# Kernel optimization log

Measured on AMD Instinct MI355X. Metric: run time of the kernel, lower is better.

The kernel has to match this reference:

```python
import jax, jax.numpy as jnp
import numpy as np
from jax import lax

B, P, ENC, H, A, E, V, TC = 64, 196, 2048, 1024, 1024, 512, 10000, 32


def setup_inputs() -> dict:
    key = jax.random.key(0)
    ks = jax.random.split(key, 24)
    s = 0.02
    inp = {
        'enc_out': jax.random.normal(ks[0], (B, P, ENC), jnp.float32),
        'enc_captions': jax.random.randint(ks[1], (B, TC), 0, V),
        'lengths': jax.random.randint(ks[2], (B,), 2, TC + 1).at[0].set(TC),
        'W_enc_att': jax.random.normal(ks[3], (A, ENC)) * s,
        'b_enc_att': jnp.zeros((A,)),
        'W_dec_att': jax.random.normal(ks[4], (A, H)) * s,
        'b_dec_att': jnp.zeros((A,)),
        'W_full': jax.random.normal(ks[5], (1, A)) * s,
        'b_full': jnp.zeros((1,)),
        'emb': jax.random.uniform(ks[6], (V, E), minval=-0.1, maxval=0.1),
        'W_ih': jax.random.normal(ks[7], (4 * H, E + ENC)) * s,
        'b_ih': jnp.zeros((4 * H,)),
        'W_hh': jax.random.normal(ks[8], (4 * H, H)) * s,
        'b_hh': jnp.zeros((4 * H,)),
        'W_init_h': jax.random.normal(ks[9], (H, ENC)) * s,
        'b_init_h': jnp.zeros((H,)),
        'W_init_c': jax.random.normal(ks[10], (H, ENC)) * s,
        'b_init_c': jnp.zeros((H,)),
        'W_beta': jax.random.normal(ks[11], (ENC, H)) * s,
        'b_beta': jnp.zeros((ENC,)),
        'W_fc': jax.random.uniform(ks[12], (V, H), minval=-0.1, maxval=0.1),
        'b_fc': jnp.zeros((V,)),
    }
    return inp


def reference(enc_out, enc_captions, lengths,
              W_enc_att, b_enc_att, W_dec_att, b_dec_att, W_full, b_full,
              emb, W_ih, b_ih, W_hh, b_hh,
              W_init_h, b_init_h, W_init_c, b_init_c,
              W_beta, b_beta, W_fc, b_fc):
    T = enc_captions.shape[1] - 1  # static max decode length (setup forces one full-length row)
    ind = jnp.argsort(-lengths)
    lens = lengths[ind]
    eo = enc_out[ind]              # [B,P,ENC] sorted by length desc
    caps = enc_captions[ind]
    dec_lens = lens - 1
    embs = emb[caps]               # [B,TC,E]

    mean_a = eo.mean(axis=1)
    h0 = mean_a @ W_init_h.T + b_init_h
    c0 = mean_a @ W_init_c.T + b_init_c

    # encoder projection is time-invariant; hoist out of the loop
    enc_att = jnp.einsum('bpe,ae->bpa', eo, W_enc_att) + b_enc_att  # [B,P,A]

    mask_ts = jnp.arange(T)[:, None] < dec_lens[None, :]            # [T,B]
    emb_ts = jnp.swapaxes(embs[:, :T, :], 0, 1)                     # [T,B,E]

    def step(carry, xs):
        h, c = carry
        emb_t, m = xs  # [B,E], [B] bool (active rows = leading batch_size_t)
        # attention
        dec = h @ W_dec_att.T + b_dec_att                            # [B,A]
        a = jax.nn.relu(enc_att + dec[:, None, :]) @ W_full[0] + b_full[0]  # [B,P]
        alpha = jax.nn.softmax(a, axis=1)
        context = jnp.einsum('bpe,bp->be', eo, alpha)                # [B,ENC]
        # gate + LSTM cell (torch gate order: i, f, g, o)
        gate = jax.nn.sigmoid(h @ W_beta.T + b_beta)
        awe = gate * context
        x = jnp.concatenate([emb_t, awe], axis=1)
        gates = x @ W_ih.T + b_ih + h @ W_hh.T + b_hh
        i, f, g, o = jnp.split(gates, 4, axis=1)
        c_new = jax.nn.sigmoid(f) * c + jax.nn.sigmoid(i) * jnp.tanh(g)
        h_new = jax.nn.sigmoid(o) * jnp.tanh(c_new)
        m2 = m[:, None]
        h2 = jnp.where(m2, h_new, h)  # inactive rows keep frozen state
        c2 = jnp.where(m2, c_new, c)
        mf = m2.astype(h.dtype)
        preds = (h_new @ W_fc.T + b_fc) * mf  # dropout = identity (eval)
        return (h2, c2), (preds, alpha * mf)

    (_, _), (preds, alphas) = lax.scan(step, (h0, c0), (emb_ts, mask_ts))
    predictions = jnp.swapaxes(preds, 0, 1)   # [B,T,V]
    alphas = jnp.swapaxes(alphas, 0, 1)       # [B,T,P]
    return predictions, alphas, caps, dec_lens, ind
```

## Files before the change

kernel.cpp:

```cpp
#include <hip/hip_runtime.h>

#define Bn   64
#define Pp   196
#define ENCd 2048
#define Hd   1024
#define Ad   1024
#define Ed   512
#define Vd   10000
#define TCd  32
#define Td   31
#define XHW  3584
#define VPAD 10240

typedef short bf16x8 __attribute__((ext_vector_type(8)));
typedef float f32x4  __attribute__((ext_vector_type(4)));

static __device__ __forceinline__ float bf2f(unsigned short u) {
    unsigned int x = ((unsigned int)u) << 16;
    float f; __builtin_memcpy(&f, &x, 4); return f;
}
static __device__ __forceinline__ unsigned short f2bf(float f) {
    unsigned int x; __builtin_memcpy(&x, &f, 4);
    x += 0x7fffu + ((x >> 16) & 1u);
    return (unsigned short)(x >> 16);
}
static __device__ __forceinline__ float sigf(float x) { return 1.f / (1.f + expf(-x)); }


__global__ void sort_kernel(const int* __restrict__ lengths, const int* __restrict__ captions,
                            int* __restrict__ ind, int* __restrict__ dl,
                            float* __restrict__ out_caps, float* __restrict__ out_dl,
                            float* __restrict__ out_ind) {
    __shared__ int s_ind[Bn];
    int tid = threadIdx.x;
    int Lt = lengths[tid];
    int pos = 0;
    for (int k = 0; k < Bn; ++k) {
        int Lk = lengths[k];
        pos += (Lk > Lt) || (Lk == Lt && k < tid);
    }
    s_ind[pos] = tid;
    __syncthreads();
    int src = s_ind[tid];
    ind[tid] = src;
    int d = lengths[src] - 1;
    dl[tid] = d;
    out_ind[tid] = (float)src;
    out_dl[tid] = (float)d;
    for (int j = 0; j < TCd; ++j)
        out_caps[tid * TCd + j] = (float)captions[src * TCd + j];
}

__global__ void cvt_kernel(const float* __restrict__ src, unsigned short* __restrict__ dst, int n) {
    int i = blockIdx.x * 256 + threadIdx.x;
    int stride = gridDim.x * 256;
    for (; i < n; i += stride) dst[i] = f2bf(src[i]);
}

__global__ void wcat_kernel(const float* __restrict__ wih, const float* __restrict__ whh,
                            unsigned short* __restrict__ wcat) {
    int j = blockIdx.y;
    int idx = blockIdx.x * 256 + threadIdx.x;
    float v = (idx < 2560) ? wih[(size_t)j * 2560 + idx] : whh[(size_t)j * 1024 + (idx - 2560)];
    wcat[(size_t)j * XHW + idx] = f2bf(v);
}

__global__ void biascat_kernel(const float* __restrict__ bih, const float* __restrict__ bhh,
                               float* __restrict__ bc) {
    int i = blockIdx.x * 256 + threadIdx.x;
    bc[i] = bih[i] + bhh[i];
}

__global__ void gather_eo_kernel(const float* __restrict__ enc_out, const int* __restrict__ ind,
                                 unsigned short* __restrict__ eo) {
    int b = blockIdx.y;
    int idx = blockIdx.x * 256 + threadIdx.x;
    int src = ind[b];
    eo[(size_t)b * (Pp * ENCd) + idx] = f2bf(enc_out[(size_t)src * (Pp * ENCd) + idx]);
}

__global__ void mean_kernel(const float* __restrict__ enc_out, const int* __restrict__ ind,
                            float* __restrict__ meanf) {
    int b = blockIdx.y;
    int e = blockIdx.x * 256 + threadIdx.x;
    int src = ind[b];
    const float* base = enc_out + (size_t)src * (Pp * ENCd) + e;
    float s = 0.f;
    for (int p = 0; p < Pp; ++p) s += base[(size_t)p * ENCd];
    meanf[b * ENCd + e] = s * (1.f / 196.f);
}

__global__ void embs_kernel(const float* __restrict__ emb, const int* __restrict__ captions,
                            const int* __restrict__ ind, unsigned short* __restrict__ xhbuf) {
    int b = blockIdx.y;
    int idx = blockIdx.x * 256 + threadIdx.x;
    int t = idx >> 9, e = idx & 511;
    int src = ind[b];
    int cap = captions[src * TCd + t];
    xhbuf[((size_t)t * Bn + b) * XHW + e] = f2bf(emb[(size_t)cap * Ed + e]);
}

__global__ void init_hc_kernel(const float* __restrict__ meanf,
                               const float* __restrict__ winh, const float* __restrict__ binh,
                               const float* __restrict__ winc, const float* __restrict__ binc,
                               unsigned short* __restrict__ xh0, float* __restrict__ cbuf) {
    int id = blockIdx.x * 256 + threadIdx.x;
    int n = id & 2047;
    int m = id >> 11;
    bool is_c = n >= 1024;
    int nn = is_c ? n - 1024 : n;
    const float* wrow = (is_c ? winc : winh) + (size_t)nn * ENCd;
    const float* arow = meanf + (size_t)m * ENCd;
    float acc = is_c ? binc[nn] : binh[nn];
    const float4* w4 = (const float4*)wrow;
    const float4* a4 = (const float4*)arow;
    for (int k = 0; k < ENCd / 4; ++k) {
        float4 wv = w4[k], av = a4[k];
        acc += wv.x * av.x + wv.y * av.y + wv.z * av.z + wv.w * av.w;
    }
    if (is_c) cbuf[(size_t)m * Hd + nn] = acc;
    else      xh0[(size_t)m * XHW + 2560 + nn] = f2bf(acc);
}

template<int MT, int NT, int EPI>
__global__ __launch_bounds__(256)
void gemm_mn(const unsigned short* __restrict__ A, int lda,
             const unsigned short* __restrict__ W,
             const float* __restrict__ bias,
             int N, int nsup, int nb, int K,
             float* __restrict__ outf, unsigned short* __restrict__ outb, int ldo,
             const int* __restrict__ dl) {
    int wave = threadIdx.x >> 6, lane = threadIdx.x & 63;
    int mt = blockIdx.x / nb;
    int nt = (blockIdx.x % nb) * 4 + wave;
    if (nt >= nsup) return;
    int m0 = mt * (MT * 16);
    int n0 = nt * (NT * 16);
    int col = lane & 15, quad = lane >> 4;

    const unsigned short* aptr = A + (size_t)(m0 + col) * lda + quad * 8;
    const unsigned short* wptr = W + (size_t)(n0 + col) * K + quad * 8;

    f32x4 acc[MT * NT];
#pragma unroll
    for (int i = 0; i < MT * NT; ++i) acc[i] = (f32x4){0.f, 0.f, 0.f, 0.f};

    for (int k = 0; k < K; k += 32) {
        bf16x8 wf[NT];
#pragma unroll
        for (int j = 0; j < NT; ++j)
            wf[j] = *(const bf16x8*)(wptr + (size_t)j * 16 * K + k);
#pragma unroll
        for (int mi = 0; mi < MT; ++mi) {
            bf16x8 af = *(const bf16x8*)(aptr + (size_t)mi * 16 * lda + k);
#pragma unroll
            for (int j = 0; j < NT; ++j)
                acc[mi * NT + j] = __builtin_amdgcn_mfma_f32_16x16x32_bf16(af, wf[j], acc[mi * NT + j], 0, 0, 0);
        }
    }

#pragma unroll
    for (int mi = 0; mi < MT; ++mi) {
#pragma unroll
        for (int r = 0; r < 4; ++r) {
            int m = m0 + mi * 16 + quad * 4 + r;
            if (EPI == 5 && m >= Td * Bn) continue;
#pragma unroll
            for (int j = 0; j < NT; ++j) {
                int n = n0 + j * 16 + col;
                if (EPI == 1) {
                    outb[(size_t)m * ldo + n] = f2bf(acc[mi * NT + j][r] + bias[n]);
                } else {
                    if (n < N) {
                        int t = m >> 6, b = m & 63;
                        float mf = (t < dl[b]) ? 1.f : 0.f;
                        float v = acc[mi * NT + j][r] + bias[n];
                        outf[((size_t)b * Td + t) * Vd + n] = v * mf;
                    }
                }
            }
        }
    }
}

template<int SK>
__global__ void gemm_sk4(const unsigned short* __restrict__ A, int lda,
                         const unsigned short* __restrict__ W,
                         int N, int K, float* __restrict__ part) {
    int wid  = (blockIdx.x * 256 + threadIdx.x) >> 6;
    int lane = threadIdx.x & 63;
    int ntiles = N >> 4;
    int s = wid / ntiles;
    int nt = wid - s * ntiles;
    int col = lane & 15, quad = lane >> 4;
    int kLen = K / SK, k0 = s * kLen;

    const unsigned short* aptr = A + (size_t)col * lda + k0 + quad * 8;
    const unsigned short* wptr = W + (size_t)(nt * 16 + col) * K + k0 + quad * 8;

    f32x4 acc[4];
#pragma unroll
    for (int i = 0; i < 4; ++i) acc[i] = (f32x4){0.f, 0.f, 0.f, 0.f};

    for (int k = 0; k < kLen; k += 32) {
        bf16x8 wf = *(const bf16x8*)(wptr + k);
#pragma unroll
        for (int mi = 0; mi < 4; ++mi) {
            bf16x8 af = *(const bf16x8*)(aptr + (size_t)mi * 16 * lda + k);
            acc[mi] = __builtin_amdgcn_mfma_f32_16x16x32_bf16(af, wf, acc[mi], 0, 0, 0);
        }
    }

    int n = nt * 16 + col;
    float* base = part + (size_t)s * Bn * N;
#pragma unroll
    for (int mi = 0; mi < 4; ++mi) {
#pragma unroll
        for (int r = 0; r < 4; ++r) {
            int m = mi * 16 + quad * 4 + r;
            base[(size_t)m * N + n] = acc[mi][r];
        }
    }
}


__global__ void scores_kernel(const float* __restrict__ pdb, const float* __restrict__ bdec,
                              const unsigned short* __restrict__ encatt,
                              const float* __restrict__ wfull,
                              float* __restrict__ scores) {
    int b = blockIdx.y;
    int tid = threadIdx.x;
    __shared__ float sdec[Ad];
    for (int i = tid; i < Ad; i += 256) {
        float v = bdec[i];
#pragma unroll
        for (int s2 = 0; s2 < 4; ++s2) v += pdb[((size_t)(s2 * Bn + b)) * 3072 + i];
        sdec[i] = v;
    }
    __syncthreads();
    int wave = tid >> 6, lane = tid & 63;
    int p = blockIdx.x * 4 + wave;
    const unsigned int* ea = (const unsigned int*)(encatt + ((size_t)(b * Pp + p) << 10));
    const float2* dp = (const float2*)sdec;
    const float2* wf = (const float2*)wfull;
    float acc = 0.f;
#pragma unroll
    for (int it = 0; it < 8; ++it) {
        int i2 = it * 64 + lane;
        unsigned int u = ea[i2];
        float2 dv = dp[i2];
        float2 wv = wf[i2];
        acc += fmaxf(bf2f((unsigned short)(u & 0xffffu)) + dv.x, 0.f) * wv.x;
        acc += fmaxf(bf2f((unsigned short)(u >> 16)) + dv.y, 0.f) * wv.y;
    }
    for (int o2 = 32; o2; o2 >>= 1) acc += __shfl_xor(acc, o2);
    if (lane == 0) scores[b * Pp + p] = acc;
}

__global__ void softmaxctx_kernel(const float* __restrict__ scores,
                                  const float* __restrict__ pdb, const float* __restrict__ bbeta,
                                  const unsigned short* __restrict__ eo,
                                  unsigned short* __restrict__ xh_t,
                                  float* __restrict__ out_alpha,
                                  const int* __restrict__ dl, int t) {
    int b = blockIdx.y, tid = threadIdx.x;
    __shared__ float red[256];
    __shared__ float sal[Pp];
    float s = (tid < Pp) ? scores[b * Pp + tid] : -1e30f;
    red[tid] = s; __syncthreads();
    for (int o2 = 128; o2; o2 >>= 1) { if (tid < o2) red[tid] = fmaxf(red[tid], red[tid + o2]); __syncthreads(); }
    float mx = red[0]; __syncthreads();
    float e = (tid < Pp) ? expf(s - mx) : 0.f;
    red[tid] = e; __syncthreads();
    for (int o2 = 128; o2; o2 >>= 1) { if (tid < o2) red[tid] += red[tid + o2]; __syncthreads(); }
    float inv = 1.f / red[0];
    if (tid < Pp) {
        float a = e * inv;
        sal[tid] = a;
        if (blockIdx.x == 0) {
            float mf = (t < dl[b]) ? 1.f : 0.f;
            out_alpha[((size_t)b * Td + t) * Pp + tid] = a * mf;
        }
    }
    __syncthreads();

    int e0 = blockIdx.x * 512 + tid * 2;
    const unsigned int* base = (const unsigned int*)(eo + (size_t)b * Pp * ENCd);
    int half = e0 >> 1;
    float a0 = 0.f, a1 = 0.f;
    for (int p = 0; p < Pp; ++p) {
        unsigned int u = base[p * (ENCd / 2) + half];
        float w = sal[p];
        a0 += w * bf2f((unsigned short)(u & 0xffffu));
        a1 += w * bf2f((unsigned short)(u >> 16));
    }
    float g0 = bbeta[e0], g1 = bbeta[e0 + 1];
#pragma unroll
    for (int s2 = 0; s2 < 4; ++s2) {
        const float* pb = pdb + ((size_t)(s2 * Bn + b)) * 3072 + Ad + e0;
        g0 += pb[0]; g1 += pb[1];
    }
    g0 = sigf(g0); g1 = sigf(g1);
    xh_t[(size_t)b * XHW + 512 + e0]     = f2bf(a0 * g0);
    xh_t[(size_t)b * XHW + 512 + e0 + 1] = f2bf(a1 * g1);
}

__global__ void lstm_kernel(const float* __restrict__ pg, const float* __restrict__ biascat,
                            float* __restrict__ c,
                            const unsigned short* __restrict__ xh_cur,
                            unsigned short* __restrict__ xh_next,
                            unsigned short* __restrict__ hall, const int* __restrict__ dl, int t) {
    int id = blockIdx.x * 256 + threadIdx.x;
    int b = id >> 10, j = id & 1023;
    float iv = biascat[j], fv = biascat[1024 + j], gv = biascat[2048 + j], ov = biascat[3072 + j];
#pragma unroll
    for (int s2 = 0; s2 < 8; ++s2) {
        const float* base = pg + ((size_t)(s2 * Bn + b)) * 4096;
        iv += base[j]; fv += base[1024 + j]; gv += base[2048 + j]; ov += base[3072 + j];
    }
    float co = c[id];
    float cn = sigf(fv) * co + sigf(iv) * tanhf(gv);
    float hn = sigf(ov) * tanhf(cn);
    bool m = t < dl[b];
    float ho = bf2f(xh_cur[(size_t)b * XHW + 2560 + j]);
    float h2 = m ? hn : ho;
    c[id] = m ? cn : co;
    xh_next[(size_t)b * XHW + 2560 + j] = f2bf(h2);
    hall[((size_t)t * Bn + b) * Hd + j] = f2bf(hn);
}


extern "C" void kernel_launch(void* const* d_in, const int* in_sizes, int n_in,
                              void* d_out, int out_size, void* d_ws, size_t ws_size,
                              hipStream_t stream) {
    const float* enc_out   = (const float*)d_in[0];
    const int*   captions  = (const int*)d_in[1];
    const int*   lengths   = (const int*)d_in[2];
    const float* W_enc_att = (const float*)d_in[3];
    const float* b_enc_att = (const float*)d_in[4];
    const float* W_dec_att = (const float*)d_in[5];
    const float* b_dec_att = (const float*)d_in[6];
    const float* W_full    = (const float*)d_in[7];
    const float* emb       = (const float*)d_in[9];
    const float* W_ih      = (const float*)d_in[10];
    const float* b_ih      = (const float*)d_in[11];
    const float* W_hh      = (const float*)d_in[12];
    const float* b_hh      = (const float*)d_in[13];
    const float* W_init_h  = (const float*)d_in[14];
    const float* b_init_h  = (const float*)d_in[15];
    const float* W_init_c  = (const float*)d_in[16];
    const float* b_init_c  = (const float*)d_in[17];
    const float* W_beta    = (const float*)d_in[18];
    const float* b_beta    = (const float*)d_in[19];
    const float* W_fc      = (const float*)d_in[20];
    const float* b_fc      = (const float*)d_in[21];

    float* out       = (float*)d_out;
    float* out_pred  = out;
    float* out_alpha = out + (size_t)Bn * Td * Vd;
    float* out_caps  = out_alpha + (size_t)Bn * Td * Pp;
    float* out_dl    = out_caps + (size_t)Bn * TCd;
    float* out_ind   = out_dl + Bn;

    char* ws = (char*)d_ws;
    size_t off = 0;
    auto take = [&](size_t n) -> char* {
        char* p = ws + off;
        off = (off + n + 255) & ~(size_t)255;
        return p;
    };
    int* ind_i   = (int*)take(Bn * 4);
    int* dl_i    = (int*)take(Bn * 4);
    unsigned short* eo_b     = (unsigned short*)take((size_t)Bn * Pp * ENCd * 2);
    unsigned short* encatt_b = (unsigned short*)take((size_t)Bn * Pp * Ad * 2);
    unsigned short* wcat_b   = (unsigned short*)take((size_t)4096 * XHW * 2);
    unsigned short* wfc_b    = (unsigned short*)take((size_t)VPAD * Hd * 2);
    unsigned short* wenc_b   = (unsigned short*)take((size_t)Ad * ENCd * 2);
    unsigned short* wdb_b    = (unsigned short*)take((size_t)3072 * Hd * 2);
    float*          biascat  = (float*)take(4096 * 4);
    float*          meanf    = (float*)take((size_t)Bn * ENCd * 4);
    unsigned short* xhbuf    = (unsigned short*)take((size_t)32 * Bn * XHW * 2);
    float*          cbuf     = (float*)take((size_t)Bn * Hd * 4);
    unsigned short* hall     = (unsigned short*)take((size_t)2048 * Hd * 2);
    float*          scores   = (float*)take((size_t)Bn * Pp * 4);
    float*          pdb      = (float*)take((size_t)4 * Bn * 3072 * 4);
    float*          pgates   = (float*)take((size_t)8 * Bn * 4096 * 4);
    (void)ws_size; (void)out_size; (void)n_in; (void)in_sizes;

    sort_kernel<<<1, 64, 0, stream>>>(lengths, captions, ind_i, dl_i, out_caps, out_dl, out_ind);

    auto cvt = [&](const float* s, unsigned short* d, int n) {
        int g = (n + 255) / 256; if (g > 4096) g = 4096;
        cvt_kernel<<<g, 256, 0, stream>>>(s, d, n);
    };
    cvt(W_enc_att, wenc_b, Ad * ENCd);
    cvt(W_dec_att, wdb_b, Ad * Hd);
    cvt(W_beta,  wdb_b + (size_t)Ad * Hd, ENCd * Hd);
    cvt(W_fc,    wfc_b,   Vd * Hd);
    wcat_kernel<<<dim3(14, 4096), 256, 0, stream>>>(W_ih, W_hh, wcat_b);
    biascat_kernel<<<16, 256, 0, stream>>>(b_ih, b_hh, biascat);

    gather_eo_kernel<<<dim3(1568, Bn), 256, 0, stream>>>(enc_out, ind_i, eo_b);
    mean_kernel<<<dim3(8, Bn), 256, 0, stream>>>(enc_out, ind_i, meanf);
    embs_kernel<<<dim3(62, Bn), 256, 0, stream>>>(emb, captions, ind_i, xhbuf);

    init_hc_kernel<<<512, 256, 0, stream>>>(meanf, W_init_h, b_init_h, W_init_c, b_init_c,
                                            xhbuf, cbuf);

    gemm_mn<8, 4, 1><<<98 * 4, 256, 0, stream>>>(eo_b, ENCd, wenc_b, b_enc_att,
        Ad, 16, 4, ENCd, nullptr, encatt_b, Ad, nullptr);

    for (int t = 0; t < Td; ++t) {
        unsigned short* xh_t = xhbuf + (size_t)t * Bn * XHW;
        unsigned short* xh_n = xhbuf + (size_t)(t + 1) * Bn * XHW;

        gemm_sk4<4><<<192, 256, 0, stream>>>(xh_t + 2560, XHW, wdb_b, 3072, Hd, pdb);

        scores_kernel<<<dim3(49, Bn), 256, 0, stream>>>(pdb, b_dec_att, encatt_b, W_full, scores);

        softmaxctx_kernel<<<dim3(4, Bn), 256, 0, stream>>>(scores, pdb, b_beta, eo_b,
            xh_t, out_alpha, dl_i, t);

        gemm_sk4<8><<<512, 256, 0, stream>>>(xh_t, XHW, wcat_b, 4096, XHW, pgates);

        lstm_kernel<<<256, 256, 0, stream>>>(pgates, biascat, cbuf, xh_t, xh_n, hall, dl_i, t);
    }

    gemm_mn<8, 4, 5><<<16 * 40, 256, 0, stream>>>(hall, Hd, wfc_b, b_fc,
        Vd, 157, 40, Hd, out_pred, nullptr, 0, dl_i);
}
```

Baseline: 2.604 ms.

## Stage GEMM tiles through LDS with a 128x128 block tile shared by four waves

```diff
diff --git a/kernel.cpp b/kernel.cpp
--- a/kernel.cpp
+++ b/kernel.cpp
@@ -25,6 +25,12 @@
     return (unsigned short)(x >> 16);
 }
 static __device__ __forceinline__ float sigf(float x) { return 1.f / (1.f + expf(-x)); }
+
+static __device__ __forceinline__ void gl_lds16(const unsigned short* g, unsigned short* l) {
+    __builtin_amdgcn_global_load_lds((const __attribute__((address_space(1))) void*)g,
+                                     (__attribute__((address_space(3))) void*)l,
+                                     16, 0, 0);
+}
 
 
 __global__ void sort_kernel(const int* __restrict__ lengths, const int* __restrict__ captions,
@@ -122,59 +128,80 @@
     else      xh0[(size_t)m * XHW + 2560 + nn] = f2bf(acc);
 }
 
-template<int MT, int NT, int EPI>
+template<int EPI>
 __global__ __launch_bounds__(256)
-void gemm_mn(const unsigned short* __restrict__ A, int lda,
-             const unsigned short* __restrict__ W,
-             const float* __restrict__ bias,
-             int N, int nsup, int nb, int K,
-             float* __restrict__ outf, unsigned short* __restrict__ outb, int ldo,
-             const int* __restrict__ dl) {
-    int wave = threadIdx.x >> 6, lane = threadIdx.x & 63;
-    int mt = blockIdx.x / nb;
-    int nt = (blockIdx.x % nb) * 4 + wave;
-    if (nt >= nsup) return;
-    int m0 = mt * (MT * 16);
-    int n0 = nt * (NT * 16);
+void gemm_tile(const unsigned short* __restrict__ A, int lda,
+               const unsigned short* __restrict__ W, int ldw,
+               const float* __restrict__ bias,
+               int N, int nbn, int K,
+               float* __restrict__ outf, unsigned short* __restrict__ outb, int ldo,
+               const int* __restrict__ dl) {
+    __shared__ unsigned short lA[128 * 32];
+    __shared__ unsigned short lB[128 * 32];
+
+    int tid  = threadIdx.x;
+    int wave = tid >> 6, lane = tid & 63;
+    int mt = blockIdx.x / nbn;
+    int nt = blockIdx.x % nbn;
+    int m0 = mt * 128, n0 = nt * 128;
+
+    int rs = lane >> 2;
+    int cs = (lane & 3) * 8;
+    const unsigned short* aG0 = A + (size_t)(m0 + wave * 16 + rs) * lda + cs;
+    const unsigned short* aG1 = aG0 + (size_t)64 * lda;
+    const unsigned short* bG0 = W + (size_t)(n0 + wave * 16 + rs) * ldw + cs;
+    const unsigned short* bG1 = bG0 + (size_t)64 * ldw;
+    unsigned short* lA0 = &lA[(wave * 16) * 32];
+    unsigned short* lA1 = &lA[(64 + wave * 16) * 32];
+    unsigned short* lB0 = &lB[(wave * 16) * 32];
+    unsigned short* lB1 = &lB[(64 + wave * 16) * 32];
+
+    int wr = wave >> 1, wc = wave & 1;
     int col = lane & 15, quad = lane >> 4;
 
-    const unsigned short* aptr = A + (size_t)(m0 + col) * lda + quad * 8;
-    const unsigned short* wptr = W + (size_t)(n0 + col) * K + quad * 8;
-
-    f32x4 acc[MT * NT];
-#pragma unroll
-    for (int i = 0; i < MT * NT; ++i) acc[i] = (f32x4){0.f, 0.f, 0.f, 0.f};
-
-    for (int k = 0; k < K; k += 32) {
-        bf16x8 wf[NT];
-#pragma unroll
-        for (int j = 0; j < NT; ++j)
-            wf[j] = *(const bf16x8*)(wptr + (size_t)j * 16 * K + k);
-#pragma unroll
-        for (int mi = 0; mi < MT; ++mi) {
-            bf16x8 af = *(const bf16x8*)(aptr + (size_t)mi * 16 * lda + k);
-#pragma unroll
-            for (int j = 0; j < NT; ++j)
-                acc[mi * NT + j] = __builtin_amdgcn_mfma_f32_16x16x32_bf16(af, wf[j], acc[mi * NT + j], 0, 0, 0);
+    f32x4 acc[4][4];
+#pragma unroll
+    for (int i = 0; i < 4; ++i)
+#pragma unroll
+        for (int j = 0; j < 4; ++j) acc[i][j] = (f32x4){0.f, 0.f, 0.f, 0.f};
+
+    for (int kt = 0; kt < K; kt += 32) {
+        __syncthreads();
+        gl_lds16(aG0 + kt, lA0);
+        gl_lds16(aG1 + kt, lA1);
+        gl_lds16(bG0 + kt, lB0);
+        gl_lds16(bG1 + kt, lB1);
+        __syncthreads();
+
+        bf16x8 af[4], bf[4];
+#pragma unroll
+        for (int i = 0; i < 4; ++i) {
+            af[i] = *(const bf16x8*)&lA[(wr * 64 + i * 16 + col) * 32 + quad * 8];
+            bf[i] = *(const bf16x8*)&lB[(wc * 64 + i * 16 + col) * 32 + quad * 8];
         }
-    }
-
-#pragma unroll
-    for (int mi = 0; mi < MT; ++mi) {
+#pragma unroll
+        for (int mi = 0; mi < 4; ++mi)
+#pragma unroll
+            for (int nj = 0; nj < 4; ++nj)
+                acc[mi][nj] = __builtin_amdgcn_mfma_f32_16x16x32_bf16(af[mi], bf[nj], acc[mi][nj], 0, 0, 0);
+    }
+
+#pragma unroll
+    for (int mi = 0; mi < 4; ++mi) {
 #pragma unroll
         for (int r = 0; r < 4; ++r) {
-            int m = m0 + mi * 16 + quad * 4 + r;
+            int m = m0 + wr * 64 + mi * 16 + quad * 4 + r;
             if (EPI == 5 && m >= Td * Bn) continue;
 #pragma unroll
-            for (int j = 0; j < NT; ++j) {
-                int n = n0 + j * 16 + col;
+            for (int nj = 0; nj < 4; ++nj) {
+                int n = n0 + wc * 64 + nj * 16 + col;
                 if (EPI == 1) {
-                    outb[(size_t)m * ldo + n] = f2bf(acc[mi * NT + j][r] + bias[n]);
+                    outb[(size_t)m * ldo + n] = f2bf(acc[mi][nj][r] + bias[n]);
                 } else {
                     if (n < N) {
                         int t = m >> 6, b = m & 63;
                         float mf = (t < dl[b]) ? 1.f : 0.f;
-                        float v = acc[mi * NT + j][r] + bias[n];
+                        float v = acc[mi][nj][r] + bias[n];
                         outf[((size_t)b * Td + t) * Vd + n] = v * mf;
                     }
                 }
@@ -407,8 +434,8 @@
     init_hc_kernel<<<512, 256, 0, stream>>>(meanf, W_init_h, b_init_h, W_init_c, b_init_c,
                                             xhbuf, cbuf);
 
-    gemm_mn<8, 4, 1><<<98 * 4, 256, 0, stream>>>(eo_b, ENCd, wenc_b, b_enc_att,
-        Ad, 16, 4, ENCd, nullptr, encatt_b, Ad, nullptr);
+    gemm_tile<1><<<98 * 8, 256, 0, stream>>>(eo_b, ENCd, wenc_b, ENCd, b_enc_att,
+        Ad, 8, ENCd, nullptr, encatt_b, Ad, nullptr);
 
     for (int t = 0; t < Td; ++t) {
         unsigned short* xh_t = xhbuf + (size_t)t * Bn * XHW;
@@ -426,6 +453,6 @@
         lstm_kernel<<<256, 256, 0, stream>>>(pgates, biascat, cbuf, xh_t, xh_n, hall, dl_i, t);
     }
 
-    gemm_mn<8, 4, 5><<<16 * 40, 256, 0, stream>>>(hall, Hd, wfc_b, b_fc,
-        Vd, 157, 40, Hd, out_pred, nullptr, 0, dl_i);
-}
+    gemm_tile<5><<<16 * 80, 256, 0, stream>>>(hall, Hd, wfc_b, Hd, b_fc,
+        Vd, 80, Hd, out_pred, nullptr, 0, dl_i);
+}
```

Measured after the change: 2.423 ms. 7.0% less time.
